# Kernel tuning notes

Hardware: AMD Instinct MI355X
Metric: run time of the kernel (lower is better)

Reference implementation:

```python
import jax, jax.numpy as jnp
import numpy as np

N_NODES = 25000
N_EDGES = 400000
N_NODE_DICT = 100
N_EDGE_DICT = 16
EMB = 128
HEADS = 4
F_OUT = 32
HF = HEADS * F_OUT  # 128
NEG_SLOPE = 0.2
LN_EPS = 1e-5


def setup_inputs() -> dict:
    key = jax.random.key(0)
    ks = jax.random.split(key, 12)
    inv_emb = 1.0 / np.sqrt(EMB)
    inputs = {
        # int graph data
        "node_features": jax.random.randint(ks[0], (N_NODES,), 0, N_NODE_DICT, dtype=jnp.int64 if jax.config.jax_enable_x64 else jnp.int32),
        "edge_features": jax.random.randint(ks[1], (N_EDGES,), 0, N_EDGE_DICT, dtype=jnp.int32),
        "edge_index": jax.random.randint(ks[2], (2, N_EDGES), 0, N_NODES, dtype=jnp.int32),
        # embedding tables (nn.Embedding ~ N(0,1))
        "node_emb": jax.random.normal(ks[3], (N_NODE_DICT, EMB), dtype=jnp.float32),
        "edge_emb": jax.random.normal(ks[4], (N_EDGE_DICT, EMB), dtype=jnp.float32),
        # target_w == neighbor_w (share_weights=True): Linear(EMB, HF)
        "W_t": jax.random.uniform(ks[5], (EMB, HF), jnp.float32, -inv_emb, inv_emb),
        "b_t": jax.random.uniform(ks[6], (HF,), jnp.float32, -inv_emb, inv_emb),
        # edgew: Linear(EMB, HF)
        "W_e": jax.random.uniform(ks[7], (EMB, HF), jnp.float32, -inv_emb, inv_emb),
        "b_e": jax.random.uniform(ks[8], (HF,), jnp.float32, -inv_emb, inv_emb),
        # attn: Linear(3*F_OUT, 1)
        "a_w": jax.random.uniform(ks[9], (3 * F_OUT,), jnp.float32, -1.0 / np.sqrt(3 * F_OUT), 1.0 / np.sqrt(3 * F_OUT)),
        "a_b": jax.random.uniform(ks[10], (), jnp.float32, -1.0 / np.sqrt(3 * F_OUT), 1.0 / np.sqrt(3 * F_OUT)),
        # LayerNorm(HF)
        "ln_gamma": jnp.ones((HF,), jnp.float32),
        "ln_beta": jnp.zeros((HF,), jnp.float32),
    }
    return inputs


def _layer_norm(x, gamma, beta):
    mu = jnp.mean(x, axis=-1, keepdims=True)
    var = jnp.mean(jnp.square(x - mu), axis=-1, keepdims=True)
    return (x - mu) * jax.lax.rsqrt(var + LN_EPS) * gamma + beta


def _forward(node_features, edge_features, edge_index,
             node_emb, edge_emb, W_t, b_t, W_e, b_e, a_w, a_b, ln_gamma, ln_beta):
    # embeddings
    h = node_emb[node_features]            # [N, EMB]
    e = edge_emb[edge_features]            # [E, EMB]

    src = edge_index[0]                    # neighbor j
    tgt = edge_index[1]                    # target i

    # per-edge projections -> [E, H, F]
    edge_h = (e @ W_e + b_e).reshape(-1, HEADS, F_OUT)
    h_proj = h @ W_t + b_t                 # project nodes once ([N, HF]) then gather
    h_i = h_proj[tgt].reshape(-1, HEADS, F_OUT)
    h_j = h_proj[src].reshape(-1, HEADS, F_OUT)  # shared weights

    # attn(cat[h_i, h_j, edge_h]) == h_i@a1 + h_j@a2 + edge_h@a3 + bias
    a1, a2, a3 = a_w[:F_OUT], a_w[F_OUT:2 * F_OUT], a_w[2 * F_OUT:]
    logits = (jnp.einsum('ehf,f->eh', h_i, a1)
              + jnp.einsum('ehf,f->eh', h_j, a2)
              + jnp.einsum('ehf,f->eh', edge_h, a3) + a_b)   # [E, H]
    eij = jnp.where(logits >= 0, logits, NEG_SLOPE * logits)  # LeakyReLU

    # scatter_softmax over edges grouped by target node
    seg_max = jax.ops.segment_max(eij, tgt, num_segments=N_NODES)   # [N, H]
    ex = jnp.exp(eij - seg_max[tgt])
    seg_sum = jax.ops.segment_sum(ex, tgt, num_segments=N_NODES)    # [N, H]
    alpha = ex / seg_sum[tgt]                                       # [E, H]

    message = alpha[:, :, None] * h_j + h_i                          # skip connection
    out = jax.ops.segment_sum(message, tgt, num_segments=N_NODES)   # [N, H, F]

    out = out.reshape(-1, HF)                                        # concat=True
    edge_out = edge_h.reshape(-1, HF)
    out = _layer_norm(out, ln_gamma, ln_beta)
    edge_out = _layer_norm(edge_out, ln_gamma, ln_beta)
    return out, edge_out


def reference(node_features, edge_features, edge_index,
              node_emb, edge_emb, W_t, b_t, W_e, b_e, a_w, a_b, ln_gamma, ln_beta):
    return _forward(node_features, edge_features, edge_index,
                    node_emb, edge_emb, W_t, b_t, W_e, b_e, a_w, a_b, ln_gamma, ln_beta)
```

## Files before the change

### kernel.cpp

```cpp
#include <hip/hip_runtime.h>
#include <hip/hip_bf16.h>

#define N_NODES 25000
#define N_EDGES 400000
#define N_NODE_DICT 100
#define N_EDGE_DICT 16
#define EMB 128
#define HF 128
#define NEG_SLOPE 0.2f
#define LN_EPS 1e-5f

#define NB 64
#define EPB (N_EDGES / NB)
#define CAP 64
#define PREB 116
#define WRB 1024
#define NODE_BLOCKS 3125

typedef __hip_bfloat16 bf16;

__device__ __forceinline__ float ldv(const void* p, int i, int m) {
    return m ? ((const float*)p)[i] : __bfloat162float(((const bf16*)p)[i]);
}

#define WS_HP   0
#define WS_S1   51200
#define WS_S2   52800
#define WS_S3   54400
#define WS_LNE  54656
#define WS_LNEF 58752
#define WS_G    66944
#define WS_B    67456
#define WS_AB   67968
#define WS_FLG  68000
#define WS_PC   68016
#define WS_BKT  6468016

__global__ __launch_bounds__(1024) void k_pre(
    const int* __restrict__ nf,
    const void* ne, const void* ee, const void* Wt, const void* bt,
    const void* We, const void* be, const void* aw, const void* gm,
    const void* bb, const void* ab,
    float* __restrict__ hp, float* __restrict__ s1, float* __restrict__ s2,
    float* __restrict__ s3, bf16* __restrict__ lne, float* __restrict__ lnef,
    float* __restrict__ gws, float* __restrict__ bws, float* __restrict__ abws,
    int* __restrict__ flg)
{
    __shared__ float hf[1024];
    __shared__ float red[2];
    __shared__ int lflg;
    int t = threadIdx.x, b = blockIdx.x;

    if (t == 0) lflg = 0;
    __syncthreads();
    {
        const unsigned short* u = (const unsigned short*)ne;
        int bad = 0;
        for (int i = t; i < N_NODE_DICT * EMB; i += 1024) {
            int ex = (u[i] >> 7) & 0xFF;
            if (ex >= 134) bad = 1;
        }
        int orv = (bad ? 1 : 0) | ((t < 200 && nf[2 * t + 1] != 0) ? 2 : 0);
        if (orv) atomicOr(&lflg, orv);
    }
    __syncthreads();
    int m = lflg & 1;
    if (b == 0 && t == 0) {
        flg[0] = lflg & 1;
        flg[1] = (lflg >> 1) & 1;
    }

    int row = b;
    int f = t & 127, kk = t >> 7;
    bool isn = row < N_NODE_DICT;
    int de = row - N_NODE_DICT;
    const void* emb = isn ? ne : ee;
    int ebase = (isn ? row : de) * EMB;
    const void* W = isn ? Wt : We;
    const void* bia = isn ? bt : be;
    float part = 0.f;
    for (int k = kk * 16; k < kk * 16 + 16; ++k)
        part += ldv(emb, ebase + k, m) * ldv(W, k * HF + f, m);
    hf[kk * 128 + f] = part;
    __syncthreads();
    float acc = 0.f;
    if (t < 128) {
        acc = ldv(bia, t, m);
        for (int q = 0; q < 8; ++q) acc += hf[q * 128 + t];
    }
    if (row == 0 && t < 128) {
        gws[t] = ldv(gm, t, m);
        bws[t] = ldv(bb, t, m);
        if (t == 0) abws[0] = ldv(ab, 0, m);
    }
    int j = t & 31, hd = (t >> 5) & 3;
    if (isn) {
        if (t < 128) {
            hp[row * HF + t] = acc;
            float p1 = acc * ldv(aw, j, m);
            float p2 = acc * ldv(aw, 32 + j, m);
            for (int s = 16; s >= 1; s >>= 1) { p1 += __shfl_xor(p1, s); p2 += __shfl_xor(p2, s); }
            if (j == 0) { s1[row * 4 + hd] = p1; s2[row * 4 + hd] = p2; }
        }
    } else {
        if (t < 128) {
            float p3 = acc * ldv(aw, 64 + j, m);
            for (int s = 16; s >= 1; s >>= 1) p3 += __shfl_xor(p3, s);
            if (j == 0) s3[de * 4 + hd] = p3;
            float tt = acc;
            for (int s = 32; s >= 1; s >>= 1) tt += __shfl_xor(tt, s);
            if ((t & 63) == 0) red[t >> 6] = tt;
        }
        __syncthreads();
        float mu = (red[0] + red[1]) * (1.0f / 128.0f);
        float d = acc - mu;
        if (t < 128) {
            float v = d * d;
            for (int s = 32; s >= 1; s >>= 1) v += __shfl_xor(v, s);
            if ((t & 63) == 0) red[t >> 6] = v;
        }
        __syncthreads();
        if (t < 128) {
            float var = (red[0] + red[1]) * (1.0f / 128.0f);
            float o = d * rsqrtf(var + LN_EPS) * ldv(gm, t, m) + ldv(bb, t, m);
            lne[de * HF + t] = __float2bfloat16(o);
            lnef[de * HF + t] = o;
        }
    }
}

__global__ __launch_bounds__(1024) void k_histwr(
    const int* __restrict__ src, const int* __restrict__ tgt,
    const int* __restrict__ ef, const int* __restrict__ nf,
    const int* __restrict__ flg, const uint4* __restrict__ lneb,
    const uint4* __restrict__ lnef4,
    unsigned int* __restrict__ pc, unsigned short* __restrict__ bkt,
    void* __restrict__ dout)
{
    __shared__ int h[N_NODES];
    __shared__ int wsum[16];
    int t = threadIdx.x, b = blockIdx.x;

    if (b < NB) {
        int w = flg[1];
        for (int i = t; i < N_NODES; i += 1024) h[i] = 0;
        __syncthreads();
        int e0 = b * EPB;
        for (int i = t; i < EPB; i += 1024) atomicAdd(&h[tgt[e0 + i]], 1);
        __syncthreads();
        const int CH = 25;
        int st = t * CH, en = st + CH;
        if (st > N_NODES) st = N_NODES;
        if (en > N_NODES) en = N_NODES;
        int ssum = 0;
        for (int i = st; i < en; ++i) ssum += h[i];
        int lane = t & 63, wv = t >> 6;
        int winc = ssum;
        for (int d = 1; d < 64; d <<= 1) { int v = __shfl_up(winc, d); if (lane >= d) winc += v; }
        if (lane == 63) wsum[wv] = winc;
        __syncthreads();
        int wbase = 0;
        for (int q = 0; q < wv; ++q) wbase += wsum[q];
        int run = wbase + winc - ssum;
        for (int i = st; i < en; ++i) {
            int c = h[i];
            pc[b * N_NODES + i] = ((unsigned)run << 16) | (unsigned)c;
            h[i] = run;
            run += c;
        }
        __syncthreads();
        for (int i = t; i < EPB; i += 1024) {
            int e = e0 + i;
            int n = tgt[e];
            int slot = atomicAdd(&h[n], 1);
            int s = src[e];
            int ds = w ? nf[s] : nf[2 * s];
            bkt[b * EPB + slot] = (unsigned short)((ds << 4) | ef[e]);
        }
    } else {
        int tid = (b - NB) * 1024 + t;
        const int stride = WRB * 1024;
        if (flg[0]) {
            uint4* out = (uint4*)((float*)dout + (size_t)N_NODES * HF);
            const int total = N_EDGES * 32;
            for (int i = tid; i < total; i += stride) {
                int e = i >> 5, c = i & 31;
                out[i] = lnef4[(ef[e] << 5) + c];
            }
        } else {
            uint4* out = (uint4*)((bf16*)dout + (size_t)N_NODES * HF);
            const int total = N_EDGES * 16;
            for (int i = tid; i < total; i += stride) {
                int e = i >> 4, c = i & 15;
                out[i] = lneb[(ef[e] << 4) + c];
            }
        }
    }
}

__global__ __launch_bounds__(512) void k_node(
    const int* __restrict__ nf, const unsigned int* __restrict__ pc,
    const unsigned short* __restrict__ bkt, const float* __restrict__ hp,
    const float* __restrict__ s1, const float* __restrict__ s2,
    const float* __restrict__ s3, const float* __restrict__ abws,
    const float* __restrict__ gws, const float* __restrict__ bws,
    void* __restrict__ dout, const int* __restrict__ flg)
{
    __shared__ unsigned short sme[8][CAP];
    __shared__ float4 smw[8][CAP];
    int w = threadIdx.x >> 6, lane = threadIdx.x & 63;
    int node = blockIdx.x * 8 + w;
    int dn = flg[1] ? nf[node] : nf[2 * node];

    unsigned int pcv = pc[lane * N_NODES + node];
    int base = (int)(pcv >> 16), c = (int)(pcv & 0xFFFFu);
    int inc = c;
    for (int d = 1; d < 64; d <<= 1) { int v = __shfl_up(inc, d); if (lane >= d) inc += v; }
    int pos = inc - c;
    int deg = __shfl(inc, 63);
    for (int j = 0; j < c; ++j) {
        int q = pos + j;
        if (q < CAP) sme[w][q] = bkt[lane * EPB + base + j];
    }
    deg = min(deg, CAP);

    float ab = abws[0];
    const float4 s1v = *(const float4*)(s1 + dn * 4);
    float l0 = -1e30f, l1 = -1e30f, l2 = -1e30f, l3 = -1e30f;
    if (lane < deg) {
        int p = sme[w][lane];
        const float4 v2 = *(const float4*)(s2 + (p >> 4) * 4);
        const float4 v3 = *(const float4*)(s3 + (p & 15) * 4);
        l0 = s1v.x + v2.x + v3.x + ab; l0 = (l0 >= 0.f) ? l0 : NEG_SLOPE * l0;
        l1 = s1v.y + v2.y + v3.y + ab; l1 = (l1 >= 0.f) ? l1 : NEG_SLOPE * l1;
        l2 = s1v.z + v2.z + v3.z + ab; l2 = (l2 >= 0.f) ? l2 : NEG_SLOPE * l2;
        l3 = s1v.w + v2.w + v3.w + ab; l3 = (l3 >= 0.f) ? l3 : NEG_SLOPE * l3;
    }
    float m0 = l0, m1 = l1, m2 = l2, m3 = l3;
    for (int q = 32; q >= 1; q >>= 1) {
        m0 = fmaxf(m0, __shfl_xor(m0, q));
        m1 = fmaxf(m1, __shfl_xor(m1, q));
        m2 = fmaxf(m2, __shfl_xor(m2, q));
        m3 = fmaxf(m3, __shfl_xor(m3, q));
    }
    float e0 = 0.f, e1 = 0.f, e2 = 0.f, e3 = 0.f;
    if (lane < deg) {
        e0 = __expf(l0 - m0); e1 = __expf(l1 - m1);
        e2 = __expf(l2 - m2); e3 = __expf(l3 - m3);
    }
    float t0 = e0, t1 = e1, t2 = e2, t3 = e3;
    for (int q = 32; q >= 1; q >>= 1) {
        t0 += __shfl_xor(t0, q); t1 += __shfl_xor(t1, q);
        t2 += __shfl_xor(t2, q); t3 += __shfl_xor(t3, q);
    }
    if (lane < deg) smw[w][lane] = make_float4(e0, e1, e2, e3);

    bool lo32 = lane < 32;
    float acc0 = 0.f, acc1 = 0.f;
    int i = 0;
    for (; i + 1 < deg; i += 2) {
        int pA = sme[w][i], pB = sme[w][i + 1];
        float4 wA = smw[w][i], wB = smw[w][i + 1];
        const float* hA = hp + (pA >> 4) * HF;
        const float* hB = hp + (pB >> 4) * HF;
        float a0 = hA[lane], b0 = hB[lane];
        float a1 = hA[64 + lane], b1 = hB[64 + lane];
        acc0 += (lo32 ? wA.x : wA.y) * a0 + (lo32 ? wB.x : wB.y) * b0;
        acc1 += (lo32 ? wA.z : wA.w) * a1 + (lo32 ? wB.z : wB.w) * b1;
    }
    if (i < deg) {
        int pA = sme[w][i];
        float4 wA = smw[w][i];
        const float* hA = hp + (pA >> 4) * HF;
        acc0 += (lo32 ? wA.x : wA.y) * hA[lane];
        acc1 += (lo32 ? wA.z : wA.w) * hA[64 + lane];
    }
    float x0 = 0.f, x1 = 0.f;
    if (deg > 0) {
        float slo = lo32 ? t0 : t1;
        float shi = lo32 ? t2 : t3;
        const float* hn = hp + dn * HF;
        x0 = acc0 / slo + (float)deg * hn[lane];
        x1 = acc1 / shi + (float)deg * hn[64 + lane];
    }
    float s = x0 + x1;
    for (int q = 32; q >= 1; q >>= 1) s += __shfl_xor(s, q);
    float mu = s * (1.0f / 128.0f);
    float d0 = x0 - mu, d1 = x1 - mu;
    float v = d0 * d0 + d1 * d1;
    for (int q = 32; q >= 1; q >>= 1) v += __shfl_xor(v, q);
    float rstd = rsqrtf(v * (1.0f / 128.0f) + LN_EPS);
    float r0 = d0 * rstd * gws[lane] + bws[lane];
    float r1 = d1 * rstd * gws[64 + lane] + bws[64 + lane];
    if (flg[0]) {
        float* o = (float*)dout;
        o[node * HF + lane] = r0;
        o[node * HF + 64 + lane] = r1;
    } else {
        bf16* o = (bf16*)dout;
        o[node * HF + lane] = __float2bfloat16(r0);
        o[node * HF + 64 + lane] = __float2bfloat16(r1);
    }
}

extern "C" void kernel_launch(void* const* d_in, const int* in_sizes, int n_in,
                              void* d_out, int out_size, void* d_ws, size_t ws_size,
                              hipStream_t stream) {
    const int* nf  = (const int*)d_in[0];
    const int* efx = (const int*)d_in[1];
    const int* ei  = (const int*)d_in[2];
    const void* node_emb = d_in[3];
    const void* edge_emb = d_in[4];
    const void* W_t = d_in[5];
    const void* b_t = d_in[6];
    const void* W_e = d_in[7];
    const void* b_e = d_in[8];
    const void* a_w = d_in[9];
    const void* a_b = d_in[10];
    const void* gmm = d_in[11];
    const void* bet = d_in[12];

    char* ws = (char*)d_ws;
    float* hp   = (float*)(ws + WS_HP);
    float* s1   = (float*)(ws + WS_S1);
    float* s2   = (float*)(ws + WS_S2);
    float* s3   = (float*)(ws + WS_S3);
    bf16*  lne  = (bf16*)(ws + WS_LNE);
    float* lnef = (float*)(ws + WS_LNEF);
    float* gws  = (float*)(ws + WS_G);
    float* bws  = (float*)(ws + WS_B);
    float* abws = (float*)(ws + WS_AB);
    int*   flg  = (int*)(ws + WS_FLG);
    unsigned int*   pc  = (unsigned int*)(ws + WS_PC);
    unsigned short* bkt = (unsigned short*)(ws + WS_BKT);

    const int* srcIdx = ei;
    const int* tgtIdx = ei + N_EDGES;

    k_pre<<<PREB, 1024, 0, stream>>>(
        nf, node_emb, edge_emb, W_t, b_t, W_e, b_e, a_w, gmm, bet, a_b,
        hp, s1, s2, s3, lne, lnef, gws, bws, abws, flg);

    k_histwr<<<NB + WRB, 1024, 0, stream>>>(
        srcIdx, tgtIdx, efx, nf, flg,
        (const uint4*)lne, (const uint4*)lnef, pc, bkt, d_out);

    k_node<<<NODE_BLOCKS, 512, 0, stream>>>(
        nf, pc, bkt, hp, s1, s2, s3, abws, gws, bws, d_out, flg);
}
```

Measured before the change: 88.33 us.

## Fuse three kernels into two and transpose bucket-offset layout for node reads

Merges the embedding-precompute kernel with the histogram/bucketing blocks into one launch, and merges the edge-output broadcast write with the per-node attention/aggregation kernel into a second launch. This removes one kernel launch and the serialization between them. The per-block offset table is stored transposed so each node block can read its 512 entries contiguously into shared memory, and the count is derived from adjacent prefix values. The histogram blocks now compute the node-feature stride flag locally instead of reading it from the precompute kernel. Edge-write blocks go from 1024-thread to 512-thread blocks with twice as many blocks.

```diff
diff --git a/kernel.cpp b/kernel.cpp
--- a/kernel.cpp
+++ b/kernel.cpp
@@ -14,7 +14,7 @@
 #define EPB (N_EDGES / NB)
 #define CAP 64
 #define PREB 116
-#define WRB 1024
+#define WRB 2048
 #define NODE_BLOCKS 3125
 
 typedef __hip_bfloat16 bf16;
@@ -36,118 +36,34 @@
 #define WS_PC   68016
 #define WS_BKT  6468016
 
-__global__ __launch_bounds__(1024) void k_pre(
-    const int* __restrict__ nf,
+__global__ __launch_bounds__(1024) void k_build(
+    const int* __restrict__ src, const int* __restrict__ tgt,
+    const int* __restrict__ ef, const int* __restrict__ nf,
     const void* ne, const void* ee, const void* Wt, const void* bt,
     const void* We, const void* be, const void* aw, const void* gm,
     const void* bb, const void* ab,
     float* __restrict__ hp, float* __restrict__ s1, float* __restrict__ s2,
     float* __restrict__ s3, bf16* __restrict__ lne, float* __restrict__ lnef,
     float* __restrict__ gws, float* __restrict__ bws, float* __restrict__ abws,
-    int* __restrict__ flg)
+    int* __restrict__ flg, unsigned int* __restrict__ pc,
+    unsigned short* __restrict__ bkt)
 {
-    __shared__ float hf[1024];
+    __shared__ int h[N_NODES];
+    __shared__ int wsum[16];
+    __shared__ int stot_s;
     __shared__ float red[2];
     __shared__ int lflg;
     int t = threadIdx.x, b = blockIdx.x;
 
-    if (t == 0) lflg = 0;
-    __syncthreads();
-    {
-        const unsigned short* u = (const unsigned short*)ne;
-        int bad = 0;
-        for (int i = t; i < N_NODE_DICT * EMB; i += 1024) {
-            int ex = (u[i] >> 7) & 0xFF;
-            if (ex >= 134) bad = 1;
-        }
-        int orv = (bad ? 1 : 0) | ((t < 200 && nf[2 * t + 1] != 0) ? 2 : 0);
-        if (orv) atomicOr(&lflg, orv);
-    }
-    __syncthreads();
-    int m = lflg & 1;
-    if (b == 0 && t == 0) {
-        flg[0] = lflg & 1;
-        flg[1] = (lflg >> 1) & 1;
-    }
-
-    int row = b;
-    int f = t & 127, kk = t >> 7;
-    bool isn = row < N_NODE_DICT;
-    int de = row - N_NODE_DICT;
-    const void* emb = isn ? ne : ee;
-    int ebase = (isn ? row : de) * EMB;
-    const void* W = isn ? Wt : We;
-    const void* bia = isn ? bt : be;
-    float part = 0.f;
-    for (int k = kk * 16; k < kk * 16 + 16; ++k)
-        part += ldv(emb, ebase + k, m) * ldv(W, k * HF + f, m);
-    hf[kk * 128 + f] = part;
-    __syncthreads();
-    float acc = 0.f;
-    if (t < 128) {
-        acc = ldv(bia, t, m);
-        for (int q = 0; q < 8; ++q) acc += hf[q * 128 + t];
-    }
-    if (row == 0 && t < 128) {
-        gws[t] = ldv(gm, t, m);
-        bws[t] = ldv(bb, t, m);
-        if (t == 0) abws[0] = ldv(ab, 0, m);
-    }
-    int j = t & 31, hd = (t >> 5) & 3;
-    if (isn) {
-        if (t < 128) {
-            hp[row * HF + t] = acc;
-            float p1 = acc * ldv(aw, j, m);
-            float p2 = acc * ldv(aw, 32 + j, m);
-            for (int s = 16; s >= 1; s >>= 1) { p1 += __shfl_xor(p1, s); p2 += __shfl_xor(p2, s); }
-            if (j == 0) { s1[row * 4 + hd] = p1; s2[row * 4 + hd] = p2; }
-        }
-    } else {
-        if (t < 128) {
-            float p3 = acc * ldv(aw, 64 + j, m);
-            for (int s = 16; s >= 1; s >>= 1) p3 += __shfl_xor(p3, s);
-            if (j == 0) s3[de * 4 + hd] = p3;
-            float tt = acc;
-            for (int s = 32; s >= 1; s >>= 1) tt += __shfl_xor(tt, s);
-            if ((t & 63) == 0) red[t >> 6] = tt;
-        }
-        __syncthreads();
-        float mu = (red[0] + red[1]) * (1.0f / 128.0f);
-        float d = acc - mu;
-        if (t < 128) {
-            float v = d * d;
-            for (int s = 32; s >= 1; s >>= 1) v += __shfl_xor(v, s);
-            if ((t & 63) == 0) red[t >> 6] = v;
-        }
-        __syncthreads();
-        if (t < 128) {
-            float var = (red[0] + red[1]) * (1.0f / 128.0f);
-            float o = d * rsqrtf(var + LN_EPS) * ldv(gm, t, m) + ldv(bb, t, m);
-            lne[de * HF + t] = __float2bfloat16(o);
-            lnef[de * HF + t] = o;
-        }
-    }
-}
-
-__global__ __launch_bounds__(1024) void k_histwr(
-    const int* __restrict__ src, const int* __restrict__ tgt,
-    const int* __restrict__ ef, const int* __restrict__ nf,
-    const int* __restrict__ flg, const uint4* __restrict__ lneb,
-    const uint4* __restrict__ lnef4,
-    unsigned int* __restrict__ pc, unsigned short* __restrict__ bkt,
-    void* __restrict__ dout)
-{
-    __shared__ int h[N_NODES];
-    __shared__ int wsum[16];
-    int t = threadIdx.x, b = blockIdx.x;
-
     if (b < NB) {
-        int w = flg[1];
+        if (t == 0) lflg = 0;
         for (int i = t; i < N_NODES; i += 1024) h[i] = 0;
         __syncthreads();
+        if (t < 200 && nf[2 * t + 1] != 0) atomicOr(&lflg, 1);
         int e0 = b * EPB;
         for (int i = t; i < EPB; i += 1024) atomicAdd(&h[tgt[e0 + i]], 1);
         __syncthreads();
+        int w = lflg;
         const int CH = 25;
         int st = t * CH, en = st + CH;
         if (st > N_NODES) st = N_NODES;
@@ -164,9 +80,16 @@
         int run = wbase + winc - ssum;
         for (int i = st; i < en; ++i) {
             int c = h[i];
-            pc[b * N_NODES + i] = ((unsigned)run << 16) | (unsigned)c;
             h[i] = run;
             run += c;
+        }
+        if (t == 0) { int s = 0; for (int q = 0; q < 16; ++q) s += wsum[q]; stot_s = s; }
+        __syncthreads();
+        for (int i = t; i < N_NODES; i += 1024) {
+            int base_i = h[i];
+            int next = (i < N_NODES - 1) ? h[i + 1] : stot_s;
+            pc[(i >> 3) * 512 + b * 8 + (i & 7)] =
+                ((unsigned)base_i << 16) | (unsigned)(next - base_i);
         }
         __syncthreads();
         for (int i = t; i < EPB; i += 1024) {
@@ -178,8 +101,102 @@
             bkt[b * EPB + slot] = (unsigned short)((ds << 4) | ef[e]);
         }
     } else {
-        int tid = (b - NB) * 1024 + t;
-        const int stride = WRB * 1024;
+        if (t == 0) lflg = 0;
+        __syncthreads();
+        {
+            const unsigned short* u = (const unsigned short*)ne;
+            int bad = 0;
+            for (int i = t; i < N_NODE_DICT * EMB; i += 1024) {
+                int ex = (u[i] >> 7) & 0xFF;
+                if (ex >= 134) bad = 1;
+            }
+            int orv = (bad ? 1 : 0) | ((t < 200 && nf[2 * t + 1] != 0) ? 2 : 0);
+            if (orv) atomicOr(&lflg, orv);
+        }
+        __syncthreads();
+        int m = lflg & 1;
+        if (b == NB && t == 0) {
+            flg[0] = lflg & 1;
+            flg[1] = (lflg >> 1) & 1;
+        }
+        int row = b - NB;
+        int f = t & 127, kk = t >> 7;
+        bool isn = row < N_NODE_DICT;
+        int de = row - N_NODE_DICT;
+        const void* emb = isn ? ne : ee;
+        int ebase = (isn ? row : de) * EMB;
+        const void* W = isn ? Wt : We;
+        const void* bia = isn ? bt : be;
+        float part = 0.f;
+        for (int k = kk * 16; k < kk * 16 + 16; ++k)
+            part += ldv(emb, ebase + k, m) * ldv(W, k * HF + f, m);
+        float* hf = (float*)h;
+        hf[kk * 128 + f] = part;
+        __syncthreads();
+        float acc = 0.f;
+        if (t < 128) {
+            acc = ldv(bia, t, m);
+            for (int q = 0; q < 8; ++q) acc += hf[q * 128 + t];
+        }
+        if (row == 0 && t < 128) {
+            gws[t] = ldv(gm, t, m);
+            bws[t] = ldv(bb, t, m);
+            if (t == 0) abws[0] = ldv(ab, 0, m);
+        }
+        int j = t & 31, hd = (t >> 5) & 3;
+        if (isn) {
+            if (t < 128) {
+                hp[row * HF + t] = acc;
+                float p1 = acc * ldv(aw, j, m);
+                float p2 = acc * ldv(aw, 32 + j, m);
+                for (int s = 16; s >= 1; s >>= 1) { p1 += __shfl_xor(p1, s); p2 += __shfl_xor(p2, s); }
+                if (j == 0) { s1[row * 4 + hd] = p1; s2[row * 4 + hd] = p2; }
+            }
+        } else {
+            if (t < 128) {
+                float p3 = acc * ldv(aw, 64 + j, m);
+                for (int s = 16; s >= 1; s >>= 1) p3 += __shfl_xor(p3, s);
+                if (j == 0) s3[de * 4 + hd] = p3;
+                float tt = acc;
+                for (int s = 32; s >= 1; s >>= 1) tt += __shfl_xor(tt, s);
+                if ((t & 63) == 0) red[t >> 6] = tt;
+            }
+            __syncthreads();
+            float mu = (red[0] + red[1]) * (1.0f / 128.0f);
+            float d = acc - mu;
+            if (t < 128) {
+                float v = d * d;
+                for (int s = 32; s >= 1; s >>= 1) v += __shfl_xor(v, s);
+                if ((t & 63) == 0) red[t >> 6] = v;
+            }
+            __syncthreads();
+            if (t < 128) {
+                float var = (red[0] + red[1]) * (1.0f / 128.0f);
+                float o = d * rsqrtf(var + LN_EPS) * ldv(gm, t, m) + ldv(bb, t, m);
+                lne[de * HF + t] = __float2bfloat16(o);
+                lnef[de * HF + t] = o;
+            }
+        }
+    }
+}
+
+__global__ __launch_bounds__(512) void k_out(
+    const int* __restrict__ nf, const unsigned int* __restrict__ pc,
+    const unsigned short* __restrict__ bkt, const float* __restrict__ hp,
+    const float* __restrict__ s1, const float* __restrict__ s2,
+    const float* __restrict__ s3, const float* __restrict__ abws,
+    const float* __restrict__ gws, const float* __restrict__ bws,
+    const int* __restrict__ ef, const uint4* __restrict__ lneb,
+    const uint4* __restrict__ lnef4,
+    void* __restrict__ dout, const int* __restrict__ flg)
+{
+    __shared__ unsigned int sm_pc[512];
+    __shared__ unsigned short sme[8][CAP];
+    __shared__ float4 smw[8][CAP];
+    int b = blockIdx.x;
+    if (b < WRB) {
+        int tid = b * 512 + threadIdx.x;
+        const int stride = WRB * 512;
         if (flg[0]) {
             uint4* out = (uint4*)((float*)dout + (size_t)N_NODES * HF);
             const int total = N_EDGES * 32;
@@ -195,111 +212,104 @@
                 out[i] = lneb[(ef[e] << 4) + c];
             }
         }
-    }
-}
-
-__global__ __launch_bounds__(512) void k_node(
-    const int* __restrict__ nf, const unsigned int* __restrict__ pc,
-    const unsigned short* __restrict__ bkt, const float* __restrict__ hp,
-    const float* __restrict__ s1, const float* __restrict__ s2,
-    const float* __restrict__ s3, const float* __restrict__ abws,
-    const float* __restrict__ gws, const float* __restrict__ bws,
-    void* __restrict__ dout, const int* __restrict__ flg)
-{
-    __shared__ unsigned short sme[8][CAP];
-    __shared__ float4 smw[8][CAP];
-    int w = threadIdx.x >> 6, lane = threadIdx.x & 63;
-    int node = blockIdx.x * 8 + w;
-    int dn = flg[1] ? nf[node] : nf[2 * node];
-
-    unsigned int pcv = pc[lane * N_NODES + node];
-    int base = (int)(pcv >> 16), c = (int)(pcv & 0xFFFFu);
-    int inc = c;
-    for (int d = 1; d < 64; d <<= 1) { int v = __shfl_up(inc, d); if (lane >= d) inc += v; }
-    int pos = inc - c;
-    int deg = __shfl(inc, 63);
-    for (int j = 0; j < c; ++j) {
-        int q = pos + j;
-        if (q < CAP) sme[w][q] = bkt[lane * EPB + base + j];
-    }
-    deg = min(deg, CAP);
-
-    float ab = abws[0];
-    const float4 s1v = *(const float4*)(s1 + dn * 4);
-    float l0 = -1e30f, l1 = -1e30f, l2 = -1e30f, l3 = -1e30f;
-    if (lane < deg) {
-        int p = sme[w][lane];
-        const float4 v2 = *(const float4*)(s2 + (p >> 4) * 4);
-        const float4 v3 = *(const float4*)(s3 + (p & 15) * 4);
-        l0 = s1v.x + v2.x + v3.x + ab; l0 = (l0 >= 0.f) ? l0 : NEG_SLOPE * l0;
-        l1 = s1v.y + v2.y + v3.y + ab; l1 = (l1 >= 0.f) ? l1 : NEG_SLOPE * l1;
-        l2 = s1v.z + v2.z + v3.z + ab; l2 = (l2 >= 0.f) ? l2 : NEG_SLOPE * l2;
-        l3 = s1v.w + v2.w + v3.w + ab; l3 = (l3 >= 0.f) ? l3 : NEG_SLOPE * l3;
-    }
-    float m0 = l0, m1 = l1, m2 = l2, m3 = l3;
-    for (int q = 32; q >= 1; q >>= 1) {
-        m0 = fmaxf(m0, __shfl_xor(m0, q));
-        m1 = fmaxf(m1, __shfl_xor(m1, q));
-        m2 = fmaxf(m2, __shfl_xor(m2, q));
-        m3 = fmaxf(m3, __shfl_xor(m3, q));
-    }
-    float e0 = 0.f, e1 = 0.f, e2 = 0.f, e3 = 0.f;
-    if (lane < deg) {
-        e0 = __expf(l0 - m0); e1 = __expf(l1 - m1);
-        e2 = __expf(l2 - m2); e3 = __expf(l3 - m3);
-    }
-    float t0 = e0, t1 = e1, t2 = e2, t3 = e3;
-    for (int q = 32; q >= 1; q >>= 1) {
-        t0 += __shfl_xor(t0, q); t1 += __shfl_xor(t1, q);
-        t2 += __shfl_xor(t2, q); t3 += __shfl_xor(t3, q);
-    }
-    if (lane < deg) smw[w][lane] = make_float4(e0, e1, e2, e3);
-
-    bool lo32 = lane < 32;
-    float acc0 = 0.f, acc1 = 0.f;
-    int i = 0;
-    for (; i + 1 < deg; i += 2) {
-        int pA = sme[w][i], pB = sme[w][i + 1];
-        float4 wA = smw[w][i], wB = smw[w][i + 1];
-        const float* hA = hp + (pA >> 4) * HF;
-        const float* hB = hp + (pB >> 4) * HF;
-        float a0 = hA[lane], b0 = hB[lane];
-        float a1 = hA[64 + lane], b1 = hB[64 + lane];
-        acc0 += (lo32 ? wA.x : wA.y) * a0 + (lo32 ? wB.x : wB.y) * b0;
-        acc1 += (lo32 ? wA.z : wA.w) * a1 + (lo32 ? wB.z : wB.w) * b1;
-    }
-    if (i < deg) {
-        int pA = sme[w][i];
-        float4 wA = smw[w][i];
-        const float* hA = hp + (pA >> 4) * HF;
-        acc0 += (lo32 ? wA.x : wA.y) * hA[lane];
-        acc1 += (lo32 ? wA.z : wA.w) * hA[64 + lane];
-    }
-    float x0 = 0.f, x1 = 0.f;
-    if (deg > 0) {
-        float slo = lo32 ? t0 : t1;
-        float shi = lo32 ? t2 : t3;
-        const float* hn = hp + dn * HF;
-        x0 = acc0 / slo + (float)deg * hn[lane];
-        x1 = acc1 / shi + (float)deg * hn[64 + lane];
-    }
-    float s = x0 + x1;
-    for (int q = 32; q >= 1; q >>= 1) s += __shfl_xor(s, q);
-    float mu = s * (1.0f / 128.0f);
-    float d0 = x0 - mu, d1 = x1 - mu;
-    float v = d0 * d0 + d1 * d1;
-    for (int q = 32; q >= 1; q >>= 1) v += __shfl_xor(v, q);
-    float rstd = rsqrtf(v * (1.0f / 128.0f) + LN_EPS);
-    float r0 = d0 * rstd * gws[lane] + bws[lane];
-    float r1 = d1 * rstd * gws[64 + lane] + bws[64 + lane];
-    if (flg[0]) {
-        float* o = (float*)dout;
-        o[node * HF + lane] = r0;
-        o[node * HF + 64 + lane] = r1;
     } else {
-        bf16* o = (bf16*)dout;
-        o[node * HF + lane] = __float2bfloat16(r0);
-        o[node * HF + 64 + lane] = __float2bfloat16(r1);
+        int nb = b - WRB;
+        int t = threadIdx.x;
+        sm_pc[t] = pc[nb * 512 + t];
+        __syncthreads();
+        int w = t >> 6, lane = t & 63;
+        int node = nb * 8 + w;
+        int dn = flg[1] ? nf[node] : nf[2 * node];
+
+        unsigned int pcv = sm_pc[lane * 8 + w];
+        int base = (int)(pcv >> 16), c = (int)(pcv & 0xFFFFu);
+        int inc = c;
+        for (int d = 1; d < 64; d <<= 1) { int v = __shfl_up(inc, d); if (lane >= d) inc += v; }
+        int pos = inc - c;
+        int deg = __shfl(inc, 63);
+        for (int j = 0; j < c; ++j) {
+            int q = pos + j;
+            if (q < CAP) sme[w][q] = bkt[lane * EPB + base + j];
+        }
+        deg = min(deg, CAP);
+
+        float ab = abws[0];
+        const float4 s1v = *(const float4*)(s1 + dn * 4);
+        float l0 = -1e30f, l1 = -1e30f, l2 = -1e30f, l3 = -1e30f;
+        if (lane < deg) {
+            int p = sme[w][lane];
+            const float4 v2 = *(const float4*)(s2 + (p >> 4) * 4);
+            const float4 v3 = *(const float4*)(s3 + (p & 15) * 4);
+            l0 = s1v.x + v2.x + v3.x + ab; l0 = (l0 >= 0.f) ? l0 : NEG_SLOPE * l0;
+            l1 = s1v.y + v2.y + v3.y + ab; l1 = (l1 >= 0.f) ? l1 : NEG_SLOPE * l1;
+            l2 = s1v.z + v2.z + v3.z + ab; l2 = (l2 >= 0.f) ? l2 : NEG_SLOPE * l2;
+            l3 = s1v.w + v2.w + v3.w + ab; l3 = (l3 >= 0.f) ? l3 : NEG_SLOPE * l3;
+        }
+        float m0 = l0, m1 = l1, m2 = l2, m3 = l3;
+        for (int q = 32; q >= 1; q >>= 1) {
+            m0 = fmaxf(m0, __shfl_xor(m0, q));
+            m1 = fmaxf(m1, __shfl_xor(m1, q));
+            m2 = fmaxf(m2, __shfl_xor(m2, q));
+            m3 = fmaxf(m3, __shfl_xor(m3, q));
+        }
+        float e0 = 0.f, e1 = 0.f, e2 = 0.f, e3 = 0.f;
+        if (lane < deg) {
+            e0 = __expf(l0 - m0); e1 = __expf(l1 - m1);
+            e2 = __expf(l2 - m2); e3 = __expf(l3 - m3);
+        }
+        float t0 = e0, t1 = e1, t2 = e2, t3 = e3;
+        for (int q = 32; q >= 1; q >>= 1) {
+            t0 += __shfl_xor(t0, q); t1 += __shfl_xor(t1, q);
+            t2 += __shfl_xor(t2, q); t3 += __shfl_xor(t3, q);
+        }
+        if (lane < deg) smw[w][lane] = make_float4(e0, e1, e2, e3);
+
+        bool lo32 = lane < 32;
+        float acc0 = 0.f, acc1 = 0.f;
+        int i = 0;
+        for (; i + 1 < deg; i += 2) {
+            int pA = sme[w][i], pB = sme[w][i + 1];
+            float4 wA = smw[w][i], wB = smw[w][i + 1];
+            const float* hA = hp + (pA >> 4) * HF;
+            const float* hB = hp + (pB >> 4) * HF;
+            float a0 = hA[lane], b0 = hB[lane];
+            float a1 = hA[64 + lane], b1 = hB[64 + lane];
+            acc0 += (lo32 ? wA.x : wA.y) * a0 + (lo32 ? wB.x : wB.y) * b0;
+            acc1 += (lo32 ? wA.z : wA.w) * a1 + (lo32 ? wB.z : wB.w) * b1;
+        }
+        if (i < deg) {
+            int pA = sme[w][i];
+            float4 wA = smw[w][i];
+            const float* hA = hp + (pA >> 4) * HF;
+            acc0 += (lo32 ? wA.x : wA.y) * hA[lane];
+            acc1 += (lo32 ? wA.z : wA.w) * hA[64 + lane];
+        }
+        float x0 = 0.f, x1 = 0.f;
+        if (deg > 0) {
+            float slo = lo32 ? t0 : t1;
+            float shi = lo32 ? t2 : t3;
+            const float* hn = hp + dn * HF;
+            x0 = acc0 / slo + (float)deg * hn[lane];
+            x1 = acc1 / shi + (float)deg * hn[64 + lane];
+        }
+        float s = x0 + x1;
+        for (int q = 32; q >= 1; q >>= 1) s += __shfl_xor(s, q);
+        float mu = s * (1.0f / 128.0f);
+        float d0 = x0 - mu, d1 = x1 - mu;
+        float v = d0 * d0 + d1 * d1;
+        for (int q = 32; q >= 1; q >>= 1) v += __shfl_xor(v, q);
+        float rstd = rsqrtf(v * (1.0f / 128.0f) + LN_EPS);
+        float r0 = d0 * rstd * gws[lane] + bws[lane];
+        float r1 = d1 * rstd * gws[64 + lane] + bws[64 + lane];
+        if (flg[0]) {
+            float* o = (float*)dout;
+            o[node * HF + lane] = r0;
+            o[node * HF + 64 + lane] = r1;
+        } else {
+            bf16* o = (bf16*)dout;
+            o[node * HF + lane] = __float2bfloat16(r0);
+            o[node * HF + 64 + lane] = __float2bfloat16(r1);
+        }
     }
 }
 
@@ -337,14 +347,12 @@
     const int* srcIdx = ei;
     const int* tgtIdx = ei + N_EDGES;
 
-    k_pre<<<PREB, 1024, 0, stream>>>(
-        nf, node_emb, edge_emb, W_t, b_t, W_e, b_e, a_w, gmm, bet, a_b,
-        hp, s1, s2, s3, lne, lnef, gws, bws, abws, flg);
-
-    k_histwr<<<NB + WRB, 1024, 0, stream>>>(
-        srcIdx, tgtIdx, efx, nf, flg,
-        (const uint4*)lne, (const uint4*)lnef, pc, bkt, d_out);
-
-    k_node<<<NODE_BLOCKS, 512, 0, stream>>>(
-        nf, pc, bkt, hp, s1, s2, s3, abws, gws, bws, d_out, flg);
+    k_build<<<NB + PREB, 1024, 0, stream>>>(
+        srcIdx, tgtIdx, efx, nf,
+        node_emb, edge_emb, W_t, b_t, W_e, b_e, a_w, gmm, bet, a_b,
+        hp, s1, s2, s3, lne, lnef, gws, bws, abws, flg, pc, bkt);
+
+    k_out<<<WRB + NODE_BLOCKS, 512, 0, stream>>>(
+        nf, pc, bkt, hp, s1, s2, s3, abws, gws, bws,
+        efx, (const uint4*)lne, (const uint4*)lnef, d_out, flg);
 }
```

New measurement: 84.71 us (median of 3 runs). 4.1% less time.
